# Kernel tuning notes

Measured on AMD Instinct MI355X. Metric: run time of the kernel, lower is better.

## Reference

```python
import jax, jax.numpy as jnp
import numpy as np

B, S, D, H = 2, 2048, 1024, 16
DH = D // H

def setup_inputs() -> dict:
    key = jax.random.key(0)
    k1, k2, k3, k4 = jax.random.split(key, 4)
    x = jax.random.normal(k1, (B, S, D), dtype=jnp.float32)
    # flax Dense kernels: [in_features, out_features]
    w_qkv = jax.random.normal(k2, (D, 3 * D), dtype=jnp.float32) / np.sqrt(D)
    w_out = jax.random.normal(k3, (D, D), dtype=jnp.float32) / np.sqrt(D)
    b_out = jax.random.normal(k4, (D,), dtype=jnp.float32) * 0.01
    return {"x": x, "w_qkv": w_qkv, "w_out": w_out, "b_out": b_out}

def reference(x, w_qkv, w_out, b_out):
    b, s, d = x.shape
    h, dh = H, d // H
    qkv = jnp.einsum('bsd,de->bse', x, w_qkv)           # [B,S,3D]
    qkv = qkv.reshape(b, s, 3, h, dh)
    qkv = jnp.transpose(qkv, (2, 0, 3, 1, 4))            # [3,B,H,S,DH]
    q, k, v = qkv[0], qkv[1], qkv[2]
    attn = jnp.einsum('bhqd,bhkd->bhqk', q, k) / jnp.sqrt(jnp.float32(dh))
    attn = jax.nn.softmax(attn, axis=-1)                 # [B,H,S,S]
    y = jnp.einsum('bhqk,bhkd->bhqd', attn, v)           # [B,H,S,DH]
    y = jnp.transpose(y, (0, 2, 1, 3)).reshape(b, s, d)  # [B,S,D]
    return jnp.einsum('bsd,de->bse', y, w_out) + b_out
```

## Files before the change

kernel.cpp:

```cpp
#include <hip/hip_runtime.h>
#include <stdint.h>

typedef __bf16 bf16_t;
typedef __bf16 bf16x8 __attribute__((ext_vector_type(8)));
typedef float f32x4 __attribute__((ext_vector_type(4)));
typedef float f32x16 __attribute__((ext_vector_type(16)));
typedef unsigned short u16;
typedef unsigned short u16x4 __attribute__((ext_vector_type(4)));
typedef unsigned short u16x8 __attribute__((ext_vector_type(8)));
typedef unsigned int u32;
typedef unsigned int u32x4 __attribute__((ext_vector_type(4)));

#define DEVI __device__ __forceinline__


DEVI u16 bits(float f) { bf16_t h = (bf16_t)f; return __builtin_bit_cast(u16, h); }

DEVI void gld16(const void* g, void* l) {
  __builtin_amdgcn_global_load_lds(
      (const __attribute__((address_space(1))) unsigned int*)g,
      (__attribute__((address_space(3))) unsigned int*)l, 16, 0, 0);
}

DEVI bf16x8 ldsr(const u16* s, int row, int cg) {
  const int byte = row * 128 + ((cg ^ (row & 7)) << 4);
  return *(const bf16x8*)((const char*)s + byte);
}

DEVI bf16x8 ldsrV(const u16* s, int row, int cg) {
  const int byte = row * 256 + ((cg ^ (row & 15)) << 4);
  return *(const bf16x8*)((const char*)s + byte);
}

DEVI float exp2v(float x) { return __builtin_amdgcn_exp2f(x); }

DEVI u32 cvtpk(float lo, float hi) {
  u32 r;
  asm("v_cvt_pk_bf16_f32 %0, %1, %2" : "=v"(r) : "v"(lo), "v"(hi));
  return r;
}

#define MFMA16(a, b, c) __builtin_amdgcn_mfma_f32_16x16x32_bf16(a, b, c, 0, 0, 0)
#define MFMA32(a, b, c) __builtin_amdgcn_mfma_f32_32x32x16_bf16(a, b, c, 0, 0, 0)

#define MKFRAG(dst, S, B)                                              \
  {                                                                    \
    u32 a_ = cvtpk(S[(B) + 0], S[(B) + 1]);                            \
    u32 b_ = cvtpk(S[(B) + 4], S[(B) + 5]);                            \
    u32 c_ = cvtpk(S[(B) + 2], S[(B) + 3]);                            \
    u32 d_ = cvtpk(S[(B) + 6], S[(B) + 7]);                            \
    asm("v_permlane32_swap_b32 %0, %1" : "+v"(a_), "+v"(b_));          \
    asm("v_permlane32_swap_b32 %0, %1" : "+v"(c_), "+v"(d_));          \
    u32x4 u_ = {a_, c_, b_, d_};                                       \
    dst = __builtin_bit_cast(bf16x8, u_);                              \
  }

__global__ void __launch_bounds__(256) prep(const float* __restrict__ x,
                                            const float* __restrict__ wqkv,
                                            const float* __restrict__ wout,
                                            u16* __restrict__ xb,
                                            u16* __restrict__ oqkv,
                                            u16* __restrict__ oout) {
  __shared__ float T[64][65];
  const int bid = blockIdx.x;
  const int tid = threadIdx.x;
  if (bid < 2048) {
    const int i = bid * 256 + tid;
    const f32x4* p = (const f32x4*)x;
    const f32x4 a = p[2 * i], b = p[2 * i + 1];
    u16x8 o;
#pragma unroll
    for (int j = 0; j < 4; ++j) { o[j] = bits(a[j]); o[4 + j] = bits(b[j]); }
    *(u16x8*)(xb + (size_t)i * 8) = o;
    return;
  }
  const int rem = bid - 2048;
  const int bx = rem & 15, byy = rem >> 4;
  const int sel = byy >= 48;
  const float* in = sel ? wout : wqkv;
  u16* out = sel ? oout : oqkv;
  const int N = sel ? 1024 : 3072;
  const int k0 = bx * 64, n0 = (sel ? byy - 48 : byy) * 64;
#pragma unroll
  for (int i = 0; i < 4; ++i) {
    const int c = i * 256 + tid;
    const int row = c >> 4, c4 = c & 15;
    const f32x4 v = *(const f32x4*)(in + (size_t)(k0 + row) * N + n0 + c4 * 4);
#pragma unroll
    for (int j = 0; j < 4; ++j) T[row][c4 * 4 + j] = v[j];
  }
  __syncthreads();
#pragma unroll
  for (int i = 0; i < 2; ++i) {
    const int c = i * 256 + tid;
    const int nrow = c >> 3, k8 = c & 7;
    u16x8 o;
#pragma unroll
    for (int j = 0; j < 8; ++j) o[j] = bits(T[k8 * 8 + j][nrow]);
    *(u16x8*)(out + (size_t)(n0 + nrow) * 1024 + k0 + k8 * 8) = o;
  }
}

template <int BN>
DEVI void gemm_core(const u16* __restrict__ A, const u16* __restrict__ Bt,
                    u16* As, u16* Bs, int m0, int n0, int Kdim,
                    f32x4 (&acc)[4][BN / 32]) {
  const int NF = BN / 32;
  const int tid = threadIdx.x;
  const int l = tid & 63, w = tid >> 6;
  const int lr = l & 15, lh = l >> 4;
  const int wr = w >> 1, wc = w & 1;
  for (int kt = 0; kt < Kdim; kt += 64) {
#pragma unroll
    for (int i = 0; i < 4; ++i) {
      const int cb = i * 256 + w * 64;
      const int c = cb + l;
      const int row = c >> 3;
      const int col = ((c & 7) ^ (row & 7)) << 3;
      gld16(A + (size_t)(m0 + row) * Kdim + kt + col, As + (size_t)cb * 8);
    }
#pragma unroll
    for (int i = 0; i < BN / 32; ++i) {
      const int cb = i * 256 + w * 64;
      const int c = cb + l;
      const int row = c >> 3;
      const int col = ((c & 7) ^ (row & 7)) << 3;
      gld16(Bt + (size_t)(n0 + row) * Kdim + kt + col, Bs + (size_t)cb * 8);
    }
    __syncthreads();
#pragma unroll
    for (int kk = 0; kk < 2; ++kk) {
      bf16x8 af[4], bfr[NF];
#pragma unroll
      for (int m = 0; m < 4; ++m) af[m] = ldsr(As, wr * 64 + m * 16 + lr, kk * 4 + lh);
#pragma unroll
      for (int n = 0; n < NF; ++n)
        bfr[n] = ldsr(Bs, wc * (BN / 2) + n * 16 + lr, kk * 4 + lh);
#pragma unroll
      for (int m = 0; m < 4; ++m)
#pragma unroll
        for (int n = 0; n < NF; ++n)
          acc[m][n] = MFMA16(af[m], bfr[n], acc[m][n]);
    }
    __syncthreads();
  }
}


DEVI void stage_half(const u16* __restrict__ G, int row0, int kt, u16* dst) {
  const int tid = threadIdx.x;
  const int l = tid & 63, wv = tid >> 6;
  const u16* gp = G + (size_t)row0 * 1024 + kt;
#pragma unroll
  for (int i = 0; i < 2; ++i) {
    const int cb = i * 512 + wv * 64;
    const int c = cb + l;
    const int rih = c >> 3;
    const int col = ((c & 7) ^ (rih & 7)) << 3;
    gld16(gp + (size_t)rih * 1024 + col, dst + cb * 8);
  }
}

template <bool SA1, bool SB2, int VM>
DEVI void qkv_tile(const u16* __restrict__ A, const u16* __restrict__ Bt,
                   int m0, int n0, int ktA1, int ktB2,
                   u16* Ac, u16* Bc, u16* An, f32x4 (&acc)[8][4]) {
  const int tid = threadIdx.x;
  const int l = tid & 63, wv = tid >> 6;
  const int lr = l & 15, lh = l >> 4;
  const int wr = wv >> 2, wc = wv & 3;
  const int ab = wr * 128, bb = wc * 64;
  bf16x8 a0[8], a1[8], b0[4], b1[4];
#pragma unroll
  for (int m = 0; m < 4; ++m)
#pragma unroll
    for (int kk = 0; kk < 2; ++kk)
      a0[m * 2 + kk] = ldsr(Ac, ab + m * 16 + lr, kk * 4 + lh);
#pragma unroll
  for (int n = 0; n < 2; ++n)
#pragma unroll
    for (int kk = 0; kk < 2; ++kk)
      b0[n * 2 + kk] = ldsr(Bc, bb + n * 16 + lr, kk * 4 + lh);
  if (SA1) stage_half(A, m0, ktA1, An);
  __builtin_amdgcn_s_barrier();
  asm volatile("s_waitcnt lgkmcnt(0)" ::: "memory");
  __builtin_amdgcn_sched_barrier(0);
  __builtin_amdgcn_s_setprio(1);
#pragma unroll
  for (int m = 0; m < 4; ++m)
#pragma unroll
    for (int n = 0; n < 2; ++n)
#pragma unroll
      for (int kk = 0; kk < 2; ++kk)
        acc[m][n] = MFMA16(a0[m * 2 + kk], b0[n * 2 + kk], acc[m][n]);
  __builtin_amdgcn_s_setprio(0);
  __builtin_amdgcn_s_barrier();
#pragma unroll
  for (int n = 0; n < 2; ++n)
#pragma unroll
    for (int kk = 0; kk < 2; ++kk)
      b1[n * 2 + kk] = ldsr(Bc, bb + 32 + n * 16 + lr, kk * 4 + lh);
  if (SA1) stage_half(A, m0 + 128, ktA1, An + 8192);
  __builtin_amdgcn_s_barrier();
  asm volatile("s_waitcnt lgkmcnt(0)" ::: "memory");
  __builtin_amdgcn_sched_barrier(0);
  __builtin_amdgcn_s_setprio(1);
#pragma unroll
  for (int m = 0; m < 4; ++m)
#pragma unroll
    for (int n = 0; n < 2; ++n)
#pragma unroll
      for (int kk = 0; kk < 2; ++kk)
        acc[m][2 + n] = MFMA16(a0[m * 2 + kk], b1[n * 2 + kk], acc[m][2 + n]);
  __builtin_amdgcn_s_setprio(0);
  __builtin_amdgcn_s_barrier();
#pragma unroll
  for (int m = 0; m < 4; ++m)
#pragma unroll
    for (int kk = 0; kk < 2; ++kk)
      a1[m * 2 + kk] = ldsr(Ac, ab + 64 + m * 16 + lr, kk * 4 + lh);
  if (SB2) stage_half(Bt, n0, ktB2, Bc);
  __builtin_amdgcn_s_barrier();
  asm volatile("s_waitcnt lgkmcnt(0)" ::: "memory");
  __builtin_amdgcn_sched_barrier(0);
  __builtin_amdgcn_s_setprio(1);
#pragma unroll
  for (int m = 0; m < 4; ++m)
#pragma unroll
    for (int n = 0; n < 2; ++n)
#pragma unroll
      for (int kk = 0; kk < 2; ++kk)
        acc[4 + m][n] = MFMA16(a1[m * 2 + kk], b0[n * 2 + kk], acc[4 + m][n]);
  __builtin_amdgcn_s_setprio(0);
  __builtin_amdgcn_s_barrier();
  if (SB2) stage_half(Bt, n0 + 128, ktB2, Bc + 8192);
  __builtin_amdgcn_s_barrier();
  __builtin_amdgcn_s_setprio(1);
#pragma unroll
  for (int m = 0; m < 4; ++m)
#pragma unroll
    for (int n = 0; n < 2; ++n)
#pragma unroll
      for (int kk = 0; kk < 2; ++kk)
        acc[4 + m][2 + n] = MFMA16(a1[m * 2 + kk], b1[n * 2 + kk], acc[4 + m][2 + n]);
  __builtin_amdgcn_s_setprio(0);
  if (VM == 4) asm volatile("s_waitcnt vmcnt(4)" ::: "memory");
  else if (VM == 0) asm volatile("s_waitcnt vmcnt(0)" ::: "memory");
  __builtin_amdgcn_s_barrier();
}

__global__ void __launch_bounds__(512, 2) gemm_qkv_k(const u16* __restrict__ A,
                                                     const u16* __restrict__ Bt,
                                                     u16* __restrict__ Qb,
                                                     u16* __restrict__ Kb,
                                                     u16* __restrict__ Vtb) {
  __shared__ u16 LA[2][16384], LB[2][16384];
  const int bid = blockIdx.x;
  const int g = bid & 7, w24 = bid >> 3;
  const int mt = (g >> 1) * 4 + (w24 & 3);
  const int nt = (g & 1) * 6 + (w24 >> 2);
  const int m0 = mt * 256, n0 = nt * 256;

  stage_half(A, m0, 0, LA[0]);
  stage_half(A, m0 + 128, 0, LA[0] + 8192);
  stage_half(Bt, n0, 0, LB[0]);
  stage_half(Bt, n0 + 128, 0, LB[0] + 8192);
  stage_half(Bt, n0, 64, LB[1]);
  stage_half(Bt, n0 + 128, 64, LB[1] + 8192);
  asm volatile("s_waitcnt vmcnt(4)" ::: "memory");
  __builtin_amdgcn_s_barrier();

  f32x4 acc[8][4] = {};
  u16 *Ac = LA[0], *Bc = LB[0], *An = LA[1], *Bn = LB[1];
#pragma unroll 1
  for (int t = 0; t < 14; ++t) {
    qkv_tile<true, true, 4>(A, Bt, m0, n0, (t + 1) * 64, (t + 2) * 64, Ac, Bc, An, acc);
    u16* tp = Ac; Ac = An; An = tp;
    tp = Bc; Bc = Bn; Bn = tp;
  }
  qkv_tile<true, false, 0>(A, Bt, m0, n0, 15 * 64, 0, Ac, Bc, An, acc);
  { u16* tp = Ac; Ac = An; An = tp; tp = Bc; Bc = Bn; Bn = tp; }
  qkv_tile<false, false, -1>(A, Bt, m0, n0, 0, 0, Ac, Bc, An, acc);

  const int tid = threadIdx.x;
  const int l = tid & 63, wv = tid >> 6;
  const int lr = l & 15, lh = l >> 4;
  const int wr = wv >> 2, wc = wv & 3;
  if (n0 >= 2048) {
    const int b = m0 >> 11, s0 = m0 & 2047;
#pragma unroll
    for (int n = 0; n < 4; ++n) {
      const int ng = n0 + wc * 64 + n * 16 + lr;
      const int h = (ng >> 6) & 15, dh = ng & 63;
      u16* vrow = Vtb + ((size_t)(b * 16 + h) * 64 + dh) * 2048 + s0;
#pragma unroll
      for (int m = 0; m < 8; ++m) {
        const int s = wr * 128 + m * 16 + lh * 4;
        u16x4 pk;
        pk[0] = bits(acc[m][n][0]);
        pk[1] = bits(acc[m][n][1]);
        pk[2] = bits(acc[m][n][2]);
        pk[3] = bits(acc[m][n][3]);
        *(u16x4*)(vrow + s) = pk;
      }
    }
  } else {
#pragma unroll
    for (int n = 0; n < 4; ++n) {
      const int ng = n0 + wc * 64 + n * 16 + lr;
      const int sel = ng >> 10, h = (ng >> 6) & 15, dh = ng & 63;
      u16* dst = sel == 0 ? Qb : Kb;
      const float qs = (sel == 0) ? 0.125f * 1.44269504f : 1.0f;
#pragma unroll
      for (int m = 0; m < 8; ++m) {
#pragma unroll
        for (int r = 0; r < 4; ++r) {
          const int mg = m0 + wr * 128 + m * 16 + lh * 4 + r;
          const int b = mg >> 11, s = mg & 2047;
          dst[((size_t)(b * 16 + h) * 2048 + s) * 64 + dh] = bits(acc[m][n][r] * qs);
        }
      }
    }
  }
}

__global__ void __launch_bounds__(256) gemm_out_k(const u16* __restrict__ A,
                                                  const u16* __restrict__ Bt,
                                                  const float* __restrict__ bias,
                                                  float* __restrict__ out) {
  __shared__ u16 As[128 * 64], Bs[128 * 64];
  const int m0 = blockIdx.y * 128, n0 = blockIdx.x * 128;
  f32x4 acc[4][4] = {};
  gemm_core<128>(A, Bt, As, Bs, m0, n0, 1024, acc);
  const int tid = threadIdx.x;
  const int l = tid & 63, w = tid >> 6;
  const int lr = l & 15, lh = l >> 4;
  const int wr = w >> 1, wc = w & 1;
#pragma unroll
  for (int n = 0; n < 4; ++n) {
    const int ng = n0 + wc * 64 + n * 16 + lr;
    const float bv = bias[ng];
#pragma unroll
    for (int m = 0; m < 4; ++m) {
#pragma unroll
      for (int r = 0; r < 4; ++r) {
        const int mg = m0 + wr * 64 + m * 16 + lh * 4 + r;
        out[(size_t)mg * 1024 + ng] = acc[m][n][r] + bv;
      }
    }
  }
}

__global__ void __launch_bounds__(512, 4) attn_k(const u16* __restrict__ Qb,
                                                 const u16* __restrict__ Kb,
                                                 const u16* __restrict__ Vt,
                                                 u16* __restrict__ Yb) {
  __shared__ char smem[65536];
  u16* const KsA = (u16*)smem;
  u16* const KsB = (u16*)(smem + 16384);
  u16* const VsA = (u16*)(smem + 32768);
  u16* const VsB = (u16*)(smem + 49152);

  const int tid = threadIdx.x;
  const int l = tid & 63, w = tid >> 6;
  const int lq = l & 31, hi = l >> 5;
  const int qw = w & 3;
  const int khalf = w >> 2;
  const int i0 = blockIdx.x;
  const int bid = (i0 & 7) * 64 + (i0 >> 3);
  const int bh = bid >> 4, qt = bid & 15;

  const u16* Qp = Qb + ((size_t)bh * 2048 + qt * 128 + qw * 32 + lq) * 64;
  bf16x8 qf0 = *(const bf16x8*)(Qp + hi * 8);
  bf16x8 qf1 = *(const bf16x8*)(Qp + 16 + hi * 8);
  bf16x8 qf2 = *(const bf16x8*)(Qp + 32 + hi * 8);
  bf16x8 qf3 = *(const bf16x8*)(Qp + 48 + hi * 8);

  const u16* Kbase = Kb + (size_t)bh * 2048 * 64;
  const u16* Vbase = Vt + (size_t)bh * 64 * 2048;

  bf16x8 ones;
#pragma unroll
  for (int j = 0; j < 8; ++j) ones[j] = (bf16_t)1.0f;

  f32x16 acc0 = {}, acc1 = {};
  f32x16 accs = {};

#define STAGE(Ksb, Vsb, kv0)                                               \
  {                                                                        \
    _Pragma("unroll") for (int ii = 0; ii < 2; ++ii) {                     \
      const int cb = ii * 512 + w * 64;                                    \
      const int c = cb + l;                                                \
      const int krow = c >> 3;                                             \
      const int kcol = ((c & 7) ^ (krow & 7)) << 3;                        \
      gld16(Kbase + (size_t)((kv0) + krow) * 64 + kcol, (Ksb) + cb * 8);   \
      const int vrow = c >> 4;                                             \
      const int vcol = ((c & 15) ^ (vrow & 15)) << 3;                      \
      gld16(Vbase + (size_t)vrow * 2048 + (kv0) + vcol, (Vsb) + cb * 8);   \
    }                                                                      \
  }

  STAGE(KsA, VsA, 0);
  asm volatile("s_waitcnt vmcnt(0)" ::: "memory");
  __builtin_amdgcn_s_barrier();

  bf16x8 pc0 = ones, pc1 = ones;
  int cur = 0;
#pragma unroll 1
  for (int t = 0; t < 16; ++t) {
    const u16* Ksc = cur ? KsB : KsA;
    const u16* Vsc = cur ? VsB : VsA;
    const u16* Vsp = cur ? VsA : VsB;

    if (t > 0) {
      __builtin_amdgcn_s_setprio(1);
      accs = MFMA32(pc0, ones, accs);
      acc0 = MFMA32(pc0, ldsrV(Vsp, lq, khalf * 8 + 4 + hi), acc0);
      acc1 = MFMA32(pc0, ldsrV(Vsp, 32 + lq, khalf * 8 + 4 + hi), acc1);
      accs = MFMA32(pc1, ones, accs);
      acc0 = MFMA32(pc1, ldsrV(Vsp, lq, khalf * 8 + 6 + hi), acc0);
      acc1 = MFMA32(pc1, ldsrV(Vsp, 32 + lq, khalf * 8 + 6 + hi), acc1);
      __builtin_amdgcn_s_setprio(0);
      asm volatile("s_waitcnt vmcnt(0)" ::: "memory");
      __builtin_amdgcn_s_barrier();
    }
    if (t + 1 < 16) STAGE((cur ? KsA : KsB), (cur ? VsA : VsB), (t + 1) * 128);

    f32x16 s0 = {}, s1 = {};
    __builtin_amdgcn_s_setprio(1);
    s0 = MFMA32(ldsr(Ksc, khalf * 64 + lq, hi), qf0, s0);
    s0 = MFMA32(ldsr(Ksc, khalf * 64 + lq, 2 + hi), qf1, s0);
    s0 = MFMA32(ldsr(Ksc, khalf * 64 + lq, 4 + hi), qf2, s0);
    s0 = MFMA32(ldsr(Ksc, khalf * 64 + lq, 6 + hi), qf3, s0);
    s1 = MFMA32(ldsr(Ksc, khalf * 64 + 32 + lq, hi), qf0, s1);
    s0[0] = exp2v(s0[0]); s0[1] = exp2v(s0[1]); s0[2] = exp2v(s0[2]); s0[3] = exp2v(s0[3]);
    s1 = MFMA32(ldsr(Ksc, khalf * 64 + 32 + lq, 2 + hi), qf1, s1);
    s0[4] = exp2v(s0[4]); s0[5] = exp2v(s0[5]); s0[6] = exp2v(s0[6]); s0[7] = exp2v(s0[7]);
    s1 = MFMA32(ldsr(Ksc, khalf * 64 + 32 + lq, 4 + hi), qf2, s1);
    s0[8] = exp2v(s0[8]); s0[9] = exp2v(s0[9]); s0[10] = exp2v(s0[10]); s0[11] = exp2v(s0[11]);
    s1 = MFMA32(ldsr(Ksc, khalf * 64 + 32 + lq, 6 + hi), qf3, s1);
    s0[12] = exp2v(s0[12]); s0[13] = exp2v(s0[13]); s0[14] = exp2v(s0[14]); s0[15] = exp2v(s0[15]);
    __builtin_amdgcn_s_setprio(0);

    bf16x8 pa0, pa1;
    MKFRAG(pa0, s0, 0);
    MKFRAG(pa1, s0, 8);

    __builtin_amdgcn_s_setprio(1);
    accs = MFMA32(pa0, ones, accs);
    s1[0] = exp2v(s1[0]); s1[1] = exp2v(s1[1]); s1[2] = exp2v(s1[2]);
    acc0 = MFMA32(pa0, ldsrV(Vsc, lq, khalf * 8 + hi), acc0);
    s1[3] = exp2v(s1[3]); s1[4] = exp2v(s1[4]); s1[5] = exp2v(s1[5]);
    acc1 = MFMA32(pa0, ldsrV(Vsc, 32 + lq, khalf * 8 + hi), acc1);
    s1[6] = exp2v(s1[6]); s1[7] = exp2v(s1[7]); s1[8] = exp2v(s1[8]);
    accs = MFMA32(pa1, ones, accs);
    s1[9] = exp2v(s1[9]); s1[10] = exp2v(s1[10]); s1[11] = exp2v(s1[11]);
    acc0 = MFMA32(pa1, ldsrV(Vsc, lq, khalf * 8 + 2 + hi), acc0);
    s1[12] = exp2v(s1[12]); s1[13] = exp2v(s1[13]); s1[14] = exp2v(s1[14]);
    acc1 = MFMA32(pa1, ldsrV(Vsc, 32 + lq, khalf * 8 + 2 + hi), acc1);
    s1[15] = exp2v(s1[15]);
    __builtin_amdgcn_s_setprio(0);

    MKFRAG(pc0, s1, 0);
    MKFRAG(pc1, s1, 8);
    cur ^= 1;
  }
  {
    const u16* Vsp = cur ? VsA : VsB;
    accs = MFMA32(pc0, ones, accs);
    acc0 = MFMA32(pc0, ldsrV(Vsp, lq, khalf * 8 + 4 + hi), acc0);
    acc1 = MFMA32(pc0, ldsrV(Vsp, 32 + lq, khalf * 8 + 4 + hi), acc1);
    accs = MFMA32(pc1, ones, accs);
    acc0 = MFMA32(pc1, ldsrV(Vsp, lq, khalf * 8 + 6 + hi), acc0);
    acc1 = MFMA32(pc1, ldsrV(Vsp, 32 + lq, khalf * 8 + 6 + hi), acc1);
  }
#undef STAGE
  __syncthreads();

  float* const F = (float*)smem;
  float* const Fp = F + (size_t)(tid & 255) * 49;
  if (khalf) {
#pragma unroll
    for (int r = 0; r < 16; ++r) {
      Fp[r] = acc0[r];
      Fp[16 + r] = acc1[r];
      Fp[32 + r] = accs[r];
    }
  }
  __syncthreads();
  if (khalf) return;
#pragma unroll
  for (int r = 0; r < 16; ++r) {
    acc0[r] += Fp[r];
    acc1[r] += Fp[16 + r];
    accs[r] += Fp[32 + r];
  }

  const int b = bh >> 4, h = bh & 15;
#pragma unroll
  for (int r = 0; r < 16; ++r) {
    const float sd = 1.0f / accs[r];
    const int row = (r & 3) + 8 * (r >> 2) + 4 * hi;
    const int sq = qt * 128 + qw * 32 + row;
    u16* yp = Yb + ((size_t)b * 2048 + sq) * 1024 + h * 64;
    yp[lq] = bits(acc0[r] * sd);
    yp[32 + lq] = bits(acc1[r] * sd);
  }
}

extern "C" void kernel_launch(void* const* d_in, const int* in_sizes, int n_in,
                              void* d_out, int out_size, void* d_ws, size_t ws_size,
                              hipStream_t stream) {
  (void)in_sizes; (void)n_in; (void)out_size; (void)ws_size;
  const float* x     = (const float*)d_in[0];
  const float* w_qkv = (const float*)d_in[1];
  const float* w_out = (const float*)d_in[2];
  const float* b_out = (const float*)d_in[3];
  float* out = (float*)d_out;

  char* ws = (char*)d_ws;
  u16* xb    = (u16*)(ws);
  u16* wqkvT = (u16*)(ws + 8388608);
  u16* woutT = (u16*)(ws + 14680064);
  u16* Qb    = (u16*)(ws + 16777216);
  u16* Kb    = (u16*)(ws + 25165824);
  u16* Vt    = (u16*)(ws + 41943040);
  u16* Yb    = xb;

  prep<<<3072, 256, 0, stream>>>(x, w_qkv, w_out, xb, wqkvT, woutT);
  gemm_qkv_k<<<192, 512, 0, stream>>>(xb, wqkvT, Qb, Kb, Vt);
  attn_k<<<512, 512, 0, stream>>>(Qb, Kb, Vt, Yb);
  gemm_out_k<<<dim3(8, 32), 256, 0, stream>>>(Yb, woutT, b_out, out);
}
```

Before: 111.1 us.

## Retile QKV GEMM to 256x192 tiles for 256 blocks

Shrinks the QKV GEMM output tile from 256x256 to 256x192, so the grid grows from 192 to 256 workgroups and lines up better with the CU count. The B staging now loads a quarter-size second half, each wave computes three 16-column fragments instead of four, and the vmcnt waits are adjusted to match. The epilogue now picks Q, K or V per column fragment, since a 192-wide tile can straddle the K/V boundary. Each tile does less MFMA work per byte loaded, in exchange for better occupancy balance across CUs.

Result: faster. 107.2 us (-3.5%).

```diff
diff --git a/kernel.cpp b/kernel.cpp
--- a/kernel.cpp
+++ b/kernel.cpp
@@ -161,16 +161,27 @@
   }
 }
 
+DEVI void stage_q(const u16* __restrict__ G, int row0, int kt, u16* dst) {
+  const int tid = threadIdx.x;
+  const int l = tid & 63, wv = tid >> 6;
+  const u16* gp = G + (size_t)row0 * 1024 + kt;
+  const int cb = wv * 64;
+  const int c = cb + l;
+  const int rih = c >> 3;
+  const int col = ((c & 7) ^ (rih & 7)) << 3;
+  gld16(gp + (size_t)rih * 1024 + col, dst + cb * 8);
+}
+
 template <bool SA1, bool SB2, int VM>
 DEVI void qkv_tile(const u16* __restrict__ A, const u16* __restrict__ Bt,
                    int m0, int n0, int ktA1, int ktB2,
-                   u16* Ac, u16* Bc, u16* An, f32x4 (&acc)[8][4]) {
+                   u16* Ac, u16* Bc, u16* An, f32x4 (&acc)[8][3]) {
   const int tid = threadIdx.x;
   const int l = tid & 63, wv = tid >> 6;
   const int lr = l & 15, lh = l >> 4;
   const int wr = wv >> 2, wc = wv & 3;
-  const int ab = wr * 128, bb = wc * 64;
-  bf16x8 a0[8], a1[8], b0[4], b1[4];
+  const int ab = wr * 128, bb = wc * 48;
+  bf16x8 a0[8], a1[8], b0[4], b1[2];
 #pragma unroll
   for (int m = 0; m < 4; ++m)
 #pragma unroll
@@ -196,10 +207,8 @@
   __builtin_amdgcn_s_setprio(0);
   __builtin_amdgcn_s_barrier();
 #pragma unroll
-  for (int n = 0; n < 2; ++n)
-#pragma unroll
-    for (int kk = 0; kk < 2; ++kk)
-      b1[n * 2 + kk] = ldsr(Bc, bb + 32 + n * 16 + lr, kk * 4 + lh);
+  for (int kk = 0; kk < 2; ++kk)
+    b1[kk] = ldsr(Bc, bb + 32 + lr, kk * 4 + lh);
   if (SA1) stage_half(A, m0 + 128, ktA1, An + 8192);
   __builtin_amdgcn_s_barrier();
   asm volatile("s_waitcnt lgkmcnt(0)" ::: "memory");
@@ -208,10 +217,8 @@
 #pragma unroll
   for (int m = 0; m < 4; ++m)
 #pragma unroll
-    for (int n = 0; n < 2; ++n)
-#pragma unroll
-      for (int kk = 0; kk < 2; ++kk)
-        acc[m][2 + n] = MFMA16(a0[m * 2 + kk], b1[n * 2 + kk], acc[m][2 + n]);
+    for (int kk = 0; kk < 2; ++kk)
+      acc[m][2] = MFMA16(a0[m * 2 + kk], b1[kk], acc[m][2]);
   __builtin_amdgcn_s_setprio(0);
   __builtin_amdgcn_s_barrier();
 #pragma unroll
@@ -233,18 +240,16 @@
         acc[4 + m][n] = MFMA16(a1[m * 2 + kk], b0[n * 2 + kk], acc[4 + m][n]);
   __builtin_amdgcn_s_setprio(0);
   __builtin_amdgcn_s_barrier();
-  if (SB2) stage_half(Bt, n0 + 128, ktB2, Bc + 8192);
+  if (SB2) stage_q(Bt, n0 + 128, ktB2, Bc + 8192);
   __builtin_amdgcn_s_barrier();
   __builtin_amdgcn_s_setprio(1);
 #pragma unroll
   for (int m = 0; m < 4; ++m)
 #pragma unroll
-    for (int n = 0; n < 2; ++n)
-#pragma unroll
-      for (int kk = 0; kk < 2; ++kk)
-        acc[4 + m][2 + n] = MFMA16(a1[m * 2 + kk], b1[n * 2 + kk], acc[4 + m][2 + n]);
+    for (int kk = 0; kk < 2; ++kk)
+      acc[4 + m][2] = MFMA16(a1[m * 2 + kk], b1[kk], acc[4 + m][2]);
   __builtin_amdgcn_s_setprio(0);
-  if (VM == 4) asm volatile("s_waitcnt vmcnt(4)" ::: "memory");
+  if (VM == 3) asm volatile("s_waitcnt vmcnt(3)" ::: "memory");
   else if (VM == 0) asm volatile("s_waitcnt vmcnt(0)" ::: "memory");
   __builtin_amdgcn_s_barrier();
 }
@@ -254,27 +259,27 @@
                                                      u16* __restrict__ Qb,
                                                      u16* __restrict__ Kb,
                                                      u16* __restrict__ Vtb) {
-  __shared__ u16 LA[2][16384], LB[2][16384];
+  __shared__ u16 LA[2][16384], LB[2][12288];
   const int bid = blockIdx.x;
-  const int g = bid & 7, w24 = bid >> 3;
-  const int mt = (g >> 1) * 4 + (w24 & 3);
-  const int nt = (g & 1) * 6 + (w24 >> 2);
-  const int m0 = mt * 256, n0 = nt * 256;
+  const int g = bid & 7, w32 = bid >> 3;
+  const int mt = g * 2 + (w32 >> 4);
+  const int nt = w32 & 15;
+  const int m0 = mt * 256, n0 = nt * 192;
 
   stage_half(A, m0, 0, LA[0]);
   stage_half(A, m0 + 128, 0, LA[0] + 8192);
   stage_half(Bt, n0, 0, LB[0]);
-  stage_half(Bt, n0 + 128, 0, LB[0] + 8192);
+  stage_q(Bt, n0 + 128, 0, LB[0] + 8192);
   stage_half(Bt, n0, 64, LB[1]);
-  stage_half(Bt, n0 + 128, 64, LB[1] + 8192);
-  asm volatile("s_waitcnt vmcnt(4)" ::: "memory");
-  __builtin_amdgcn_s_barrier();
-
-  f32x4 acc[8][4] = {};
+  stage_q(Bt, n0 + 128, 64, LB[1] + 8192);
+  asm volatile("s_waitcnt vmcnt(3)" ::: "memory");
+  __builtin_amdgcn_s_barrier();
+
+  f32x4 acc[8][3] = {};
   u16 *Ac = LA[0], *Bc = LB[0], *An = LA[1], *Bn = LB[1];
 #pragma unroll 1
   for (int t = 0; t < 14; ++t) {
-    qkv_tile<true, true, 4>(A, Bt, m0, n0, (t + 1) * 64, (t + 2) * 64, Ac, Bc, An, acc);
+    qkv_tile<true, true, 3>(A, Bt, m0, n0, (t + 1) * 64, (t + 2) * 64, Ac, Bc, An, acc);
     u16* tp = Ac; Ac = An; An = tp;
     tp = Bc; Bc = Bn; Bn = tp;
   }
@@ -286,12 +291,12 @@
   const int l = tid & 63, wv = tid >> 6;
   const int lr = l & 15, lh = l >> 4;
   const int wr = wv >> 2, wc = wv & 3;
-  if (n0 >= 2048) {
-    const int b = m0 >> 11, s0 = m0 & 2047;
-#pragma unroll
-    for (int n = 0; n < 4; ++n) {
-      const int ng = n0 + wc * 64 + n * 16 + lr;
-      const int h = (ng >> 6) & 15, dh = ng & 63;
+  const int b = m0 >> 11, s0 = m0 & 2047;
+#pragma unroll
+  for (int n = 0; n < 3; ++n) {
+    const int ng = n0 + wc * 48 + n * 16 + lr;
+    const int sel = ng >> 10, h = (ng >> 6) & 15, dh = ng & 63;
+    if (sel == 2) {
       u16* vrow = Vtb + ((size_t)(b * 16 + h) * 64 + dh) * 2048 + s0;
 #pragma unroll
       for (int m = 0; m < 8; ++m) {
@@ -303,12 +308,7 @@
         pk[3] = bits(acc[m][n][3]);
         *(u16x4*)(vrow + s) = pk;
       }
-    }
-  } else {
-#pragma unroll
-    for (int n = 0; n < 4; ++n) {
-      const int ng = n0 + wc * 64 + n * 16 + lr;
-      const int sel = ng >> 10, h = (ng >> 6) & 15, dh = ng & 63;
+    } else {
       u16* dst = sel == 0 ? Qb : Kb;
       const float qs = (sel == 0) ? 0.125f * 1.44269504f : 1.0f;
 #pragma unroll
@@ -316,8 +316,8 @@
 #pragma unroll
         for (int r = 0; r < 4; ++r) {
           const int mg = m0 + wr * 128 + m * 16 + lh * 4 + r;
-          const int b = mg >> 11, s = mg & 2047;
-          dst[((size_t)(b * 16 + h) * 2048 + s) * 64 + dh] = bits(acc[m][n][r] * qs);
+          const int b2 = mg >> 11, s = mg & 2047;
+          dst[((size_t)(b2 * 16 + h) * 2048 + s) * 64 + dh] = bits(acc[m][n][r] * qs);
         }
       }
     }
@@ -528,7 +528,7 @@
   u16* Yb    = xb;
 
   prep<<<3072, 256, 0, stream>>>(x, w_qkv, w_out, xb, wqkvT, woutT);
-  gemm_qkv_k<<<192, 512, 0, stream>>>(xb, wqkvT, Qb, Kb, Vt);
+  gemm_qkv_k<<<256, 512, 0, stream>>>(xb, wqkvT, Qb, Kb, Vt);
   attn_k<<<512, 512, 0, stream>>>(Qb, Kb, Vt, Yb);
   gemm_out_k<<<dim3(8, 32), 256, 0, stream>>>(Yb, woutT, b_out, out);
 }
```
